# Optimization experiments

Measured on AMD Instinct MI355X. Metric: run time of the kernel, lower is better.

## Reference

```python
import jax, jax.numpy as jnp
from jax import lax
import numpy as np

DIM = 256
D_STATE = 16
D_CONV = 4
EXPAND = 2
D_INNER = EXPAND * DIM          # 512
DT_RANK = (DIM + 15) // 16      # 16
EPS = 1e-5


def setup_inputs() -> dict:
    key = jax.random.key(0)
    ks = jax.random.split(key, 8)
    B, H, W = 8, 32, 32
    dt_init = 0.01  # softplus(b_dt) ~= dt_init at init (mamba-style)
    return {
        "x": jax.random.normal(ks[0], (B, DIM, H, W), jnp.float32),
        "ln_gamma": jnp.ones((DIM,), jnp.float32),
        "ln_beta": jnp.zeros((DIM,), jnp.float32),
        "W_in": jax.random.normal(ks[1], (DIM, 2 * D_INNER), jnp.float32) * 0.02,
        "conv_w": jax.random.normal(ks[2], (D_INNER, D_CONV), jnp.float32) * 0.2,
        "conv_b": jnp.zeros((D_INNER,), jnp.float32),
        "W_xproj": jax.random.normal(ks[3], (D_INNER, DT_RANK + 2 * D_STATE), jnp.float32) * 0.02,
        "W_dt": jax.random.normal(ks[4], (DT_RANK, D_INNER), jnp.float32) * 0.05,
        "b_dt": jnp.full((D_INNER,), float(np.log(np.expm1(dt_init))), jnp.float32),
        "A_log": jnp.log(jnp.broadcast_to(
            jnp.arange(1, D_STATE + 1, dtype=jnp.float32), (D_INNER, D_STATE))),
        "D_skip": jnp.ones((D_INNER,), jnp.float32),
        "W_out": jax.random.normal(ks[5], (D_INNER, DIM), jnp.float32) * 0.02,
    }


def _mamba_layer(x, ln_gamma, ln_beta, W_in, conv_w, conv_b, W_xproj,
                 W_dt, b_dt, A_log, D_skip, W_out):
    B, C, H, W = x.shape
    L = H * W
    # (B,C,H,W) -> (B, L, C)
    xf = x.transpose(0, 2, 3, 1).reshape(B, L, C)
    # LayerNorm over channel dim
    mu = xf.mean(-1, keepdims=True)
    var = ((xf - mu) ** 2).mean(-1, keepdims=True)
    xn = (xf - mu) * lax.rsqrt(var + EPS) * ln_gamma + ln_beta
    # in_proj -> u (ssm branch) and z (gate branch)
    xz = xn @ W_in                              # [B, L, 2*D_INNER]
    u, z = xz[..., :D_INNER], xz[..., D_INNER:]
    # causal depthwise conv1d over L, then SiLU
    uc = u.transpose(0, 2, 1)                   # [B, D_INNER, L]
    uc = lax.conv_general_dilated(
        uc, conv_w[:, None, :], window_strides=(1,),
        padding=[(D_CONV - 1, 0)], feature_group_count=D_INNER)
    u2 = jax.nn.silu(uc + conv_b[None, :, None]).transpose(0, 2, 1)  # [B, L, D_INNER]
    # input-dependent dt, B, C
    dbc = u2 @ W_xproj                          # [B, L, DT_RANK + 2*D_STATE]
    dt = jax.nn.softplus(dbc[..., :DT_RANK] @ W_dt + b_dt)            # [B, L, D_INNER]
    Bm = dbc[..., DT_RANK:DT_RANK + D_STATE]    # [B, L, D_STATE]
    Cm = dbc[..., DT_RANK + D_STATE:]           # [B, L, D_STATE]
    A = -jnp.exp(A_log)                         # [D_INNER, D_STATE]

    def step(h, ins):
        dt_t, B_t, C_t, u_t = ins               # [B,Din], [B,S], [B,S], [B,Din]
        dA = jnp.exp(dt_t[:, :, None] * A)      # [B, Din, S]
        h = dA * h + dt_t[:, :, None] * B_t[:, None, :] * u_t[:, :, None]
        y = jnp.einsum('bds,bs->bd', h, C_t)
        return h, y

    h0 = jnp.zeros((B, D_INNER, D_STATE), xf.dtype)
    xs = (dt.transpose(1, 0, 2), Bm.transpose(1, 0, 2),
          Cm.transpose(1, 0, 2), u2.transpose(1, 0, 2))
    _, ys = lax.scan(step, h0, xs)              # ys: [L, B, D_INNER]
    y = ys.transpose(1, 0, 2) + u2 * D_skip     # skip connection D*u
    y = y * jax.nn.silu(z)                      # gate
    o = y @ W_out                               # [B, L, C]
    return o.reshape(B, H, W, C).transpose(0, 3, 1, 2) + x


def reference(x, ln_gamma, ln_beta, W_in, conv_w, conv_b, W_xproj,
              W_dt, b_dt, A_log, D_skip, W_out):
    return _mamba_layer(x, ln_gamma, ln_beta, W_in, conv_w, conv_b, W_xproj,
                        W_dt, b_dt, A_log, D_skip, W_out)
```

## Files before the change

### kernel.cpp

```cpp
#include <hip/hip_runtime.h>
#include <hip/hip_bf16.h>
#include <math.h>

#define DIMC   256
#define DI     512
#define DS     16
#define DTR    16
#define NX     48
#define BATCH  8
#define LSEQ   1024
#define MROWS  8192
#define CHUNK  64
#define NC     (LSEQ / CHUNK)

typedef __attribute__((ext_vector_type(8))) short short8;
typedef __attribute__((ext_vector_type(4))) float f32x4;

__device__ __forceinline__ unsigned short f2bf(float v) {
  __hip_bfloat16 h = __float2bfloat16(v);
  return *reinterpret_cast<unsigned short*>(&h);
}

__device__ __forceinline__ float dpp_sum16(float v) {
  float t;
  t = __int_as_float(__builtin_amdgcn_mov_dpp(__float_as_int(v), 0xB1,  0xF, 0xF, true)); v += t;
  t = __int_as_float(__builtin_amdgcn_mov_dpp(__float_as_int(v), 0x4E,  0xF, 0xF, true)); v += t;
  t = __int_as_float(__builtin_amdgcn_mov_dpp(__float_as_int(v), 0x141, 0xF, 0xF, true)); v += t;
  t = __int_as_float(__builtin_amdgcn_mov_dpp(__float_as_int(v), 0x140, 0xF, 0xF, true)); v += t;
  return v;
}

__global__ __launch_bounds__(256) void prologue(const float* __restrict__ W_in,
                                                const float* __restrict__ W_out,
                                                const float* __restrict__ W_xproj,
                                                const float* __restrict__ W_dt,
                                                const float* __restrict__ x,
                                                const float* __restrict__ gamma,
                                                const float* __restrict__ beta,
                                                unsigned short* __restrict__ Wib,
                                                unsigned short* __restrict__ Wob,
                                                unsigned short* __restrict__ Wxpb,
                                                unsigned short* __restrict__ Wdtb,
                                                unsigned short* __restrict__ xnb) {
  __shared__ float sx[DIMC][67];
  __shared__ float smean[64], srs[64];
  const int blk = blockIdx.x, tid = threadIdx.x;
  if (blk < 384) {
    float (*t)[67] = sx;
    const float* W; unsigned short* Wt; int K, N, bx, by;
    if (blk < 256) { W = W_in;  Wt = Wib; K = DIMC; N = 1024; bx = blk & 31; by = blk >> 5; }
    else           { W = W_out; Wt = Wob; K = DI;   N = DIMC; bx = (blk - 256) & 7; by = (blk - 256) >> 3; }
    int n0 = bx * 32, k0 = by * 32;
    int tx = tid & 31, ty = tid >> 5;
    for (int i = ty; i < 32; i += 8) t[i][tx] = W[(size_t)(k0 + i) * N + n0 + tx];
    __syncthreads();
    for (int i = ty; i < 32; i += 8)
      Wt[(size_t)(n0 + i) * K + k0 + tx] = f2bf(t[tx][i]);
    return;
  }
  if (blk < 512) {
    int idx = (blk - 384) * 256 + tid;
    int n = idx >> 9, k = idx & 511;
    Wxpb[idx] = (n < NX) ? f2bf(W_xproj[(size_t)k * NX + n]) : (unsigned short)0;
    return;
  }
  if (blk < 576) {
    int idx = (blk - 512) * 256 + tid;
    int n = idx >> 5, k = idx & 31;
    Wdtb[idx] = (k < DTR) ? f2bf(W_dt[(size_t)k * DI + n]) : (unsigned short)0;
    return;
  }
  const int lb = blk - 576;
  const int b = lb >> 4, l0 = (lb & 15) * 64;
  {
    const int cbase = tid >> 2;
    const int lp = (tid & 3) * 16;
#pragma unroll
    for (int cg = 0; cg < 4; ++cg) {
      const int c = cg * 64 + cbase;
      const float* p = x + ((size_t)b * DIMC + c) * LSEQ + l0 + lp;
#pragma unroll
      for (int q = 0; q < 4; ++q) {
        float4 v = *(const float4*)(p + q * 4);
        sx[c][lp + q * 4 + 0] = v.x;
        sx[c][lp + q * 4 + 1] = v.y;
        sx[c][lp + q * 4 + 2] = v.z;
        sx[c][lp + q * 4 + 3] = v.w;
      }
    }
  }
  __syncthreads();
  {
    const int lane = tid & 63, w = tid >> 6;
    const int l = (w << 4) + (lane & 15);
    const int quad = lane >> 4;
    float sum = 0.f, sq = 0.f;
#pragma unroll 8
    for (int cc = 0; cc < 64; ++cc) {
      float v = sx[quad * 64 + cc][l];
      sum += v; sq += v * v;
    }
    sum += __shfl_xor(sum, 16); sq += __shfl_xor(sq, 16);
    sum += __shfl_xor(sum, 32); sq += __shfl_xor(sq, 32);
    if (quad == 0) {
      float mean = sum * (1.f / 256.f);
      float var  = sq * (1.f / 256.f) - mean * mean;
      smean[l] = mean; srs[l] = rsqrtf(var + 1e-5f);
    }
  }
  __syncthreads();
  {
    const float gg = gamma[tid], bb = beta[tid];
    const size_t base = ((size_t)b * LSEQ + l0) * DIMC + tid;
#pragma unroll 4
    for (int ll = 0; ll < 64; ++ll) {
      float v = (sx[tid][ll] - smean[ll]) * srs[ll] * gg + bb;
      xnb[base + (size_t)ll * DIMC] = f2bf(v);
    }
  }
}

#define GTM 128
#define GTN 64
#define GBK 32
__global__ __launch_bounds__(256) void gemm_bf16(const unsigned short* __restrict__ A,
                                                 const unsigned short* __restrict__ Bt,
                                                 float* __restrict__ C,
                                                 int M, int N, int K, int mode,
                                                 const float* __restrict__ X) {
  __shared__ unsigned short As[GTM][GBK];
  __shared__ unsigned short Bs[GTN][GBK];
  const int tid = threadIdx.x;
  const int lane = tid & 63, wave = tid >> 6;
  const int wm = wave >> 1, wn = wave & 1;
  const int quad = lane >> 4, l16 = lane & 15;
  const int m0 = blockIdx.y * GTM, n0 = blockIdx.x * GTN;

  f32x4 acc[4][2];
#pragma unroll
  for (int i = 0; i < 4; ++i)
#pragma unroll
    for (int j = 0; j < 2; ++j) acc[i][j] = (f32x4){0.f, 0.f, 0.f, 0.f};

  for (int k0 = 0; k0 < K; k0 += GBK) {
#pragma unroll
    for (int q = 0; q < 2; ++q) {
      int id = q * 256 + tid;
      int row = id >> 2, c = id & 3;
      uint4 v = *(const uint4*)(A + (size_t)(m0 + row) * K + k0 + c * 8);
      *(uint4*)&As[row][c * 8] = v;
    }
    {
      int row = tid >> 2, c = tid & 3;
      uint4 v = *(const uint4*)(Bt + (size_t)(n0 + row) * K + k0 + c * 8);
      *(uint4*)&Bs[row][c * 8] = v;
    }
    __syncthreads();
    short8 af[4], bfrag[2];
#pragma unroll
    for (int i = 0; i < 4; ++i)
      af[i] = *(const short8*)&As[wm * 64 + i * 16 + l16][quad * 8];
#pragma unroll
    for (int j = 0; j < 2; ++j)
      bfrag[j] = *(const short8*)&Bs[wn * 32 + j * 16 + l16][quad * 8];
#pragma unroll
    for (int i = 0; i < 4; ++i)
#pragma unroll
      for (int j = 0; j < 2; ++j)
        acc[i][j] = __builtin_amdgcn_mfma_f32_16x16x32_bf16(af[i], bfrag[j], acc[i][j], 0, 0, 0);
    __syncthreads();
  }

  if (mode == 0) {
#pragma unroll
    for (int i = 0; i < 4; ++i) {
      int rowb = wm * 64 + i * 16 + quad * 4;
#pragma unroll
      for (int j = 0; j < 2; ++j) {
        int n = n0 + wn * 32 + j * 16 + l16;
#pragma unroll
        for (int r = 0; r < 4; ++r)
          C[(size_t)(m0 + rowb + r) * N + n] = acc[i][j][r];
      }
    }
  } else {
#pragma unroll
    for (int i = 0; i < 4; ++i) {
      int m = m0 + wm * 64 + i * 16 + quad * 4;
      int b = m >> 10, l = m & 1023;
#pragma unroll
      for (int j = 0; j < 2; ++j) {
        int n = n0 + wn * 32 + j * 16 + l16;
        size_t o = (size_t)b * (DIMC * LSEQ) + (size_t)n * LSEQ + l;
        f32x4 xv = *(const f32x4*)(X + o);
        f32x4 rv = acc[i][j] + xv;
        *(f32x4*)(C + o) = rv;
      }
    }
  }
}

__global__ __launch_bounds__(256) void conv_silu(const float* __restrict__ xz,
                                                 const float* __restrict__ conv_w,
                                                 const float* __restrict__ conv_b,
                                                 float* __restrict__ u2,
                                                 unsigned int* __restrict__ u2b) {
  int idx = (blockIdx.x * 256 + threadIdx.x) * 2;
  int c = idx & (DI - 1);
  int m = idx >> 9;
  int l = m & 1023;
  float2 acc = *(const float2*)(conv_b + c);
  float4 w0 = *(const float4*)(conv_w + c * 4);
  float4 w1 = *(const float4*)(conv_w + c * 4 + 4);
  const float wa[4] = {w0.x, w0.y, w0.z, w0.w};
  const float wb[4] = {w1.x, w1.y, w1.z, w1.w};
#pragma unroll
  for (int k = 0; k < 4; ++k) {
    int lj = l - 3 + k;
    if (lj >= 0) {
      float2 v = *(const float2*)(xz + (size_t)(m - 3 + k) * 1024 + c);
      acc.x = fmaf(v.x, wa[k], acc.x);
      acc.y = fmaf(v.y, wb[k], acc.y);
    }
  }
  float vx = acc.x / (1.f + __expf(-acc.x));
  float vy = acc.y / (1.f + __expf(-acc.y));
  *(float2*)(u2 + idx) = make_float2(vx, vy);
  u2b[idx >> 1] = (unsigned int)f2bf(vx) | ((unsigned int)f2bf(vy) << 16);
}

__global__ __launch_bounds__(256) void xproj_dt(const unsigned short* __restrict__ u2b,
                                                const unsigned short* __restrict__ Wxpb,
                                                const unsigned short* __restrict__ Wdtb,
                                                const float* __restrict__ b_dt,
                                                float* __restrict__ dbc64,
                                                float* __restrict__ dtv) {
  __shared__ unsigned short Bs[64][512 + 8];
  __shared__ unsigned short sdbc[32][40];
  const int m0 = blockIdx.x * 32;
  const int tid = threadIdx.x, lane = tid & 63, w = tid >> 6;
  const int quad = lane >> 4, l16 = lane & 15;
#pragma unroll
  for (int q = 0; q < 16; ++q) {
    int id = q * 256 + tid;
    int row = id >> 6, c8 = id & 63;
    *(uint4*)&Bs[row][c8 * 8] = *(const uint4*)(Wxpb + (size_t)row * 512 + c8 * 8);
  }
  __syncthreads();
  f32x4 acc[2];
  acc[0] = (f32x4){0.f, 0.f, 0.f, 0.f};
  acc[1] = (f32x4){0.f, 0.f, 0.f, 0.f};
#pragma unroll 4
  for (int k0 = 0; k0 < 512; k0 += 32) {
    short8 af0 = *(const short8*)(u2b + (size_t)(m0 + l16) * 512 + k0 + quad * 8);
    short8 af1 = *(const short8*)(u2b + (size_t)(m0 + 16 + l16) * 512 + k0 + quad * 8);
    short8 bf  = *(const short8*)&Bs[w * 16 + l16][k0 + quad * 8];
    acc[0] = __builtin_amdgcn_mfma_f32_16x16x32_bf16(af0, bf, acc[0], 0, 0, 0);
    acc[1] = __builtin_amdgcn_mfma_f32_16x16x32_bf16(af1, bf, acc[1], 0, 0, 0);
  }
#pragma unroll
  for (int i = 0; i < 2; ++i)
#pragma unroll
    for (int r = 0; r < 4; ++r)
      dbc64[(size_t)(m0 + i * 16 + quad * 4 + r) * 64 + w * 16 + l16] = acc[i][r];
  if (w < 2) {
#pragma unroll
    for (int i = 0; i < 2; ++i)
#pragma unroll
      for (int r = 0; r < 4; ++r)
        sdbc[i * 16 + quad * 4 + r][w * 16 + l16] = f2bf(acc[i][r]);
  }
  __syncthreads();
  short8 af0 = *(const short8*)&sdbc[l16][quad * 8];
  short8 af1 = *(const short8*)&sdbc[16 + l16][quad * 8];
#pragma unroll
  for (int jn = 0; jn < 8; ++jn) {
    const int n0 = w * 128 + jn * 16;
    short8 bf = *(const short8*)(Wdtb + (size_t)(n0 + l16) * 32 + quad * 8);
    f32x4 a0 = (f32x4){0.f, 0.f, 0.f, 0.f}, a1 = a0;
    a0 = __builtin_amdgcn_mfma_f32_16x16x32_bf16(af0, bf, a0, 0, 0, 0);
    a1 = __builtin_amdgcn_mfma_f32_16x16x32_bf16(af1, bf, a1, 0, 0, 0);
    const float bd = b_dt[n0 + l16];
#pragma unroll
    for (int r = 0; r < 4; ++r) {
      float v = a0[r] + bd;
      dtv[(size_t)(m0 + quad * 4 + r) * DI + n0 + l16] = (v > 20.f) ? v : log1pf(__expf(v));
      float v2 = a1[r] + bd;
      dtv[(size_t)(m0 + 16 + quad * 4 + r) * DI + n0 + l16] = (v2 > 20.f) ? v2 : log1pf(__expf(v2));
    }
  }
}

__global__ __launch_bounds__(256) void scan_pass1(const float* __restrict__ dtv,
                                                  const float* __restrict__ u2,
                                                  const float* __restrict__ dbc64,
                                                  const float* __restrict__ A_log,
                                                  float* __restrict__ hend,
                                                  float* __restrict__ Ssum) {
  const int bb = blockIdx.x, dblk = blockIdx.y, cc = blockIdx.z;
  const int tid = threadIdx.x;
  const int di = tid >> 4, s = tid & 15;
  const int d = dblk * 16 + di;
  const float Ads = -__expf(A_log[d * DS + s]);

  __shared__ float2 sdu[CHUNK][16];
  __shared__ float  sB[CHUNK][16];
  {
    const int t0 = cc * CHUNK;
#pragma unroll
    for (int q = 0; q < 4; ++q) {
      int lin = q * 256 + tid;
      int tt = lin >> 4, dd = lin & 15;
      size_t m = (size_t)bb * LSEQ + t0 + tt;
      sdu[tt][dd] = make_float2(dtv[m * DI + dblk * 16 + dd], u2[m * DI + dblk * 16 + dd]);
      sB[tt][dd]  = dbc64[m * 64 + DTR + dd];
    }
  }
  __syncthreads();
  float h = 0.f, dtsum = 0.f;
#pragma unroll 4
  for (int tt = 0; tt < CHUNK; ++tt) {
    float2 du = sdu[tt][di];
    float Bv  = sB[tt][s];
    h = fmaf(__expf(du.x * Ads), h, du.x * du.y * Bv);
    dtsum += du.x;
  }
  size_t ci = ((size_t)(bb * NC + cc) * DI + d);
  hend[ci * DS + s] = h;
  if (s == 0) Ssum[ci] = dtsum;
}

__global__ __launch_bounds__(256) void scan_pass3(const float* __restrict__ dtv,
                                                  const float* __restrict__ u2,
                                                  const float* __restrict__ dbc64,
                                                  const float* __restrict__ xz,
                                                  const float* __restrict__ A_log,
                                                  const float* __restrict__ D_skip,
                                                  const float* __restrict__ hend,
                                                  const float* __restrict__ Ssum,
                                                  unsigned short* __restrict__ yb) {
  const int bb = blockIdx.x, dblk = blockIdx.y, cc = blockIdx.z;
  const int tid = threadIdx.x;
  const int di = tid >> 4, s = tid & 15;
  const int d = dblk * 16 + di;
  const float Ads = -__expf(A_log[d * DS + s]);

  __shared__ float2 sdu[CHUNK][16];
  __shared__ float2 sBC[CHUNK][16];
  __shared__ float  sz[CHUNK][16], sy[CHUNK][16];
  const int t0 = cc * CHUNK;
#pragma unroll
  for (int q = 0; q < 4; ++q) {
    int lin = q * 256 + tid;
    int tt = lin >> 4, dd = lin & 15;
    size_t m = (size_t)bb * LSEQ + t0 + tt;
    sdu[tt][dd] = make_float2(dtv[m * DI + dblk * 16 + dd], u2[m * DI + dblk * 16 + dd]);
    sBC[tt][dd] = make_float2(dbc64[m * 64 + DTR + dd], dbc64[m * 64 + DTR + DS + dd]);
    sz [tt][dd] = xz[m * 1024 + DI + dblk * 16 + dd];
  }
  float h = 0.f;
  for (int j = 0; j < cc; ++j) {
    size_t cj = ((size_t)(bb * NC + j) * DI + d);
    h = fmaf(__expf(Ads * Ssum[cj]), h, hend[cj * DS + s]);
  }
  __syncthreads();
#pragma unroll 4
  for (int tt = 0; tt < CHUNK; ++tt) {
    float2 du = sdu[tt][di];
    float2 bc = sBC[tt][s];
    h = fmaf(__expf(du.x * Ads), h, du.x * du.y * bc.x);
    float v = dpp_sum16(h * bc.y);
    if (s == 0) sy[tt][di] = v;
  }
  __syncthreads();
#pragma unroll
  for (int q = 0; q < 4; ++q) {
    int lin = q * 256 + tid;
    int tt = lin >> 4, dd = lin & 15;
    size_t m = (size_t)bb * LSEQ + t0 + tt;
    float yv = sy[tt][dd] + sdu[tt][dd].y * D_skip[dblk * 16 + dd];
    float z = sz[tt][dd];
    yv *= z / (1.f + __expf(-z));
    yb[m * DI + dblk * 16 + dd] = f2bf(yv);
  }
}

extern "C" void kernel_launch(void* const* d_in, const int* in_sizes, int n_in,
                              void* d_out, int out_size, void* d_ws, size_t ws_size,
                              hipStream_t stream) {
  const float* x       = (const float*)d_in[0];
  const float* ln_g    = (const float*)d_in[1];
  const float* ln_b    = (const float*)d_in[2];
  const float* W_in    = (const float*)d_in[3];
  const float* conv_w  = (const float*)d_in[4];
  const float* conv_b  = (const float*)d_in[5];
  const float* W_xproj = (const float*)d_in[6];
  const float* W_dt    = (const float*)d_in[7];
  const float* b_dt    = (const float*)d_in[8];
  const float* A_log   = (const float*)d_in[9];
  const float* D_skip  = (const float*)d_in[10];
  const float* W_out   = (const float*)d_in[11];
  float* out = (float*)d_out;

  float* ws    = (float*)d_ws;
  float* xz    = ws;
  float* u2    = xz   + (size_t)MROWS * 1024;
  float* dbc64 = u2   + (size_t)MROWS * DI;
  float* dtv   = dbc64 + (size_t)MROWS * 64;
  float* hend  = dtv  + (size_t)MROWS * DI;
  float* Ssum  = hend + (size_t)BATCH * NC * DI * DS;
  unsigned short* u2b  = (unsigned short*)(Ssum + (size_t)BATCH * NC * DI);
  unsigned short* yb   = u2b + (size_t)MROWS * DI;
  unsigned short* xnb  = yb;
  unsigned short* Wib  = yb  + (size_t)MROWS * DI;
  unsigned short* Wob  = Wib + (size_t)DIMC * 1024;
  unsigned short* Wxpb = Wob + (size_t)DI * DIMC;
  unsigned short* Wdtb = Wxpb + (size_t)64 * 512;

  prologue<<<704, 256, 0, stream>>>(W_in, W_out, W_xproj, W_dt, x, ln_g, ln_b,
                                    Wib, Wob, Wxpb, Wdtb, xnb);

  gemm_bf16<<<dim3(1024 / GTN, MROWS / GTM), 256, 0, stream>>>(
      xnb, Wib, xz, MROWS, 1024, DIMC, 0, nullptr);

  conv_silu<<<(MROWS * DI) / 512, 256, 0, stream>>>(xz, conv_w, conv_b, u2,
                                                    (unsigned int*)u2b);

  xproj_dt<<<MROWS / 32, 256, 0, stream>>>(u2b, Wxpb, Wdtb, b_dt, dbc64, dtv);

  dim3 gp13(BATCH, DI / 16, NC);
  scan_pass1<<<gp13, 256, 0, stream>>>(dtv, u2, dbc64, A_log, hend, Ssum);
  scan_pass3<<<gp13, 256, 0, stream>>>(dtv, u2, dbc64, xz, A_log, D_skip,
                                       hend, Ssum, yb);

  gemm_bf16<<<dim3(DIMC / GTN, MROWS / GTM), 256, 0, stream>>>(
      yb, Wob, out, MROWS, DIMC, DI, 1, x);
}
```

Measured before the change: 216.7 us.

## Store xz and u2 in bf16 and add a separate inter-chunk scan pass

The in_proj GEMM now writes xz as bf16 rather than fp32, and the fp32 copy of u2 is dropped; conv, scan_pass1 and scan_pass3 read the bf16 buffers and widen them to float. A new scan_pass2 kernel walks the chunks once per (batch, channel) to produce the incoming state for each chunk, so scan_pass3 no longer repeats an O(cc) prefix loop over earlier chunk summaries in every block. This cuts intermediate memory traffic and redundant serial work, at the cost of one extra kernel launch and lower precision for u, z and the skip term.

```diff
diff --git a/kernel.cpp b/kernel.cpp
--- a/kernel.cpp
+++ b/kernel.cpp
@@ -19,6 +19,9 @@
 __device__ __forceinline__ unsigned short f2bf(float v) {
   __hip_bfloat16 h = __float2bfloat16(v);
   return *reinterpret_cast<unsigned short*>(&h);
+}
+__device__ __forceinline__ float bf2f(unsigned short u) {
+  return __int_as_float(((int)u) << 16);
 }
 
 __device__ __forceinline__ float dpp_sum16(float v) {
@@ -125,7 +128,7 @@
 #define GBK 32
 __global__ __launch_bounds__(256) void gemm_bf16(const unsigned short* __restrict__ A,
                                                  const unsigned short* __restrict__ Bt,
-                                                 float* __restrict__ C,
+                                                 void* __restrict__ Cout,
                                                  int M, int N, int K, int mode,
                                                  const float* __restrict__ X) {
   __shared__ unsigned short As[GTM][GBK];
@@ -171,7 +174,8 @@
     __syncthreads();
   }
 
-  if (mode == 0) {
+  if (mode == 2) {
+    unsigned short* Cb = (unsigned short*)Cout;
 #pragma unroll
     for (int i = 0; i < 4; ++i) {
       int rowb = wm * 64 + i * 16 + quad * 4;
@@ -180,10 +184,11 @@
         int n = n0 + wn * 32 + j * 16 + l16;
 #pragma unroll
         for (int r = 0; r < 4; ++r)
-          C[(size_t)(m0 + rowb + r) * N + n] = acc[i][j][r];
+          Cb[(size_t)(m0 + rowb + r) * N + n] = f2bf(acc[i][j][r]);
       }
     }
   } else {
+    float* C = (float*)Cout;
 #pragma unroll
     for (int i = 0; i < 4; ++i) {
       int m = m0 + wm * 64 + i * 16 + quad * 4;
@@ -200,10 +205,9 @@
   }
 }
 
-__global__ __launch_bounds__(256) void conv_silu(const float* __restrict__ xz,
+__global__ __launch_bounds__(256) void conv_silu(const unsigned short* __restrict__ xzb,
                                                  const float* __restrict__ conv_w,
                                                  const float* __restrict__ conv_b,
-                                                 float* __restrict__ u2,
                                                  unsigned int* __restrict__ u2b) {
   int idx = (blockIdx.x * 256 + threadIdx.x) * 2;
   int c = idx & (DI - 1);
@@ -218,14 +222,13 @@
   for (int k = 0; k < 4; ++k) {
     int lj = l - 3 + k;
     if (lj >= 0) {
-      float2 v = *(const float2*)(xz + (size_t)(m - 3 + k) * 1024 + c);
-      acc.x = fmaf(v.x, wa[k], acc.x);
-      acc.y = fmaf(v.y, wb[k], acc.y);
+      unsigned int v = *(const unsigned int*)(xzb + (size_t)(m - 3 + k) * 1024 + c);
+      acc.x = fmaf(bf2f((unsigned short)(v & 0xffff)), wa[k], acc.x);
+      acc.y = fmaf(bf2f((unsigned short)(v >> 16)),   wb[k], acc.y);
     }
   }
   float vx = acc.x / (1.f + __expf(-acc.x));
   float vy = acc.y / (1.f + __expf(-acc.y));
-  *(float2*)(u2 + idx) = make_float2(vx, vy);
   u2b[idx >> 1] = (unsigned int)f2bf(vx) | ((unsigned int)f2bf(vy) << 16);
 }
 
@@ -292,7 +295,7 @@
 }
 
 __global__ __launch_bounds__(256) void scan_pass1(const float* __restrict__ dtv,
-                                                  const float* __restrict__ u2,
+                                                  const unsigned short* __restrict__ u2b,
                                                   const float* __restrict__ dbc64,
                                                   const float* __restrict__ A_log,
                                                   float* __restrict__ hend,
@@ -312,7 +315,8 @@
       int lin = q * 256 + tid;
       int tt = lin >> 4, dd = lin & 15;
       size_t m = (size_t)bb * LSEQ + t0 + tt;
-      sdu[tt][dd] = make_float2(dtv[m * DI + dblk * 16 + dd], u2[m * DI + dblk * 16 + dd]);
+      sdu[tt][dd] = make_float2(dtv[m * DI + dblk * 16 + dd],
+                                bf2f(u2b[m * DI + dblk * 16 + dd]));
       sB[tt][dd]  = dbc64[m * 64 + DTR + dd];
     }
   }
@@ -330,14 +334,30 @@
   if (s == 0) Ssum[ci] = dtsum;
 }
 
+__global__ __launch_bounds__(256) void scan_pass2(const float* __restrict__ A_log,
+                                                  const float* __restrict__ hend,
+                                                  const float* __restrict__ Ssum,
+                                                  float* __restrict__ hin) {
+  const int bb = blockIdx.x, dblk = blockIdx.y;
+  const int tid = threadIdx.x;
+  const int di = tid >> 4, s = tid & 15;
+  const int d = dblk * 16 + di;
+  const float Ads = -__expf(A_log[d * DS + s]);
+  float h = 0.f;
+  for (int cc = 0; cc < NC; ++cc) {
+    size_t ci = ((size_t)(bb * NC + cc) * DI + d);
+    hin[ci * DS + s] = h;
+    h = fmaf(__expf(Ads * Ssum[ci]), h, hend[ci * DS + s]);
+  }
+}
+
 __global__ __launch_bounds__(256) void scan_pass3(const float* __restrict__ dtv,
-                                                  const float* __restrict__ u2,
+                                                  const unsigned short* __restrict__ u2b,
                                                   const float* __restrict__ dbc64,
-                                                  const float* __restrict__ xz,
+                                                  const unsigned short* __restrict__ xzb,
                                                   const float* __restrict__ A_log,
                                                   const float* __restrict__ D_skip,
-                                                  const float* __restrict__ hend,
-                                                  const float* __restrict__ Ssum,
+                                                  const float* __restrict__ hin,
                                                   unsigned short* __restrict__ yb) {
   const int bb = blockIdx.x, dblk = blockIdx.y, cc = blockIdx.z;
   const int tid = threadIdx.x;
@@ -354,16 +374,13 @@
     int lin = q * 256 + tid;
     int tt = lin >> 4, dd = lin & 15;
     size_t m = (size_t)bb * LSEQ + t0 + tt;
-    sdu[tt][dd] = make_float2(dtv[m * DI + dblk * 16 + dd], u2[m * DI + dblk * 16 + dd]);
+    sdu[tt][dd] = make_float2(dtv[m * DI + dblk * 16 + dd],
+                              bf2f(u2b[m * DI + dblk * 16 + dd]));
     sBC[tt][dd] = make_float2(dbc64[m * 64 + DTR + dd], dbc64[m * 64 + DTR + DS + dd]);
-    sz [tt][dd] = xz[m * 1024 + DI + dblk * 16 + dd];
-  }
-  float h = 0.f;
-  for (int j = 0; j < cc; ++j) {
-    size_t cj = ((size_t)(bb * NC + j) * DI + d);
-    h = fmaf(__expf(Ads * Ssum[cj]), h, hend[cj * DS + s]);
-  }
-  __syncthreads();
+    sz [tt][dd] = bf2f(xzb[m * 1024 + DI + dblk * 16 + dd]);
+  }
+  __syncthreads();
+  float h = hin[((size_t)(bb * NC + cc) * DI + d) * DS + s];
 #pragma unroll 4
   for (int tt = 0; tt < CHUNK; ++tt) {
     float2 du = sdu[tt][di];
@@ -403,13 +420,13 @@
   float* out = (float*)d_out;
 
   float* ws    = (float*)d_ws;
-  float* xz    = ws;
-  float* u2    = xz   + (size_t)MROWS * 1024;
-  float* dbc64 = u2   + (size_t)MROWS * DI;
+  float* dbc64 = ws;
   float* dtv   = dbc64 + (size_t)MROWS * 64;
   float* hend  = dtv  + (size_t)MROWS * DI;
-  float* Ssum  = hend + (size_t)BATCH * NC * DI * DS;
-  unsigned short* u2b  = (unsigned short*)(Ssum + (size_t)BATCH * NC * DI);
+  float* hin   = hend + (size_t)BATCH * NC * DI * DS;
+  float* Ssum  = hin  + (size_t)BATCH * NC * DI * DS;
+  unsigned short* xzb  = (unsigned short*)(Ssum + (size_t)BATCH * NC * DI);
+  unsigned short* u2b  = xzb + (size_t)MROWS * 1024;
   unsigned short* yb   = u2b + (size_t)MROWS * DI;
   unsigned short* xnb  = yb;
   unsigned short* Wib  = yb  + (size_t)MROWS * DI;
@@ -421,17 +438,18 @@
                                     Wib, Wob, Wxpb, Wdtb, xnb);
 
   gemm_bf16<<<dim3(1024 / GTN, MROWS / GTM), 256, 0, stream>>>(
-      xnb, Wib, xz, MROWS, 1024, DIMC, 0, nullptr);
-
-  conv_silu<<<(MROWS * DI) / 512, 256, 0, stream>>>(xz, conv_w, conv_b, u2,
+      xnb, Wib, xzb, MROWS, 1024, DIMC, 2, nullptr);
+
+  conv_silu<<<(MROWS * DI) / 512, 256, 0, stream>>>(xzb, conv_w, conv_b,
                                                     (unsigned int*)u2b);
 
   xproj_dt<<<MROWS / 32, 256, 0, stream>>>(u2b, Wxpb, Wdtb, b_dt, dbc64, dtv);
 
   dim3 gp13(BATCH, DI / 16, NC);
-  scan_pass1<<<gp13, 256, 0, stream>>>(dtv, u2, dbc64, A_log, hend, Ssum);
-  scan_pass3<<<gp13, 256, 0, stream>>>(dtv, u2, dbc64, xz, A_log, D_skip,
-                                       hend, Ssum, yb);
+  dim3 gp2(BATCH, DI / 16);
+  scan_pass1<<<gp13, 256, 0, stream>>>(dtv, u2b, dbc64, A_log, hend, Ssum);
+  scan_pass2<<<gp2, 256, 0, stream>>>(A_log, hend, Ssum, hin);
+  scan_pass3<<<gp13, 256, 0, stream>>>(dtv, u2b, dbc64, xzb, A_log, D_skip, hin, yb);
 
   gemm_bf16<<<dim3(DIMC / GTN, MROWS / GTM), 256, 0, stream>>>(
       yb, Wob, out, MROWS, DIMC, DI, 1, x);
```

Result: faster. 205.5 us (-5.2%).
